# Kernel optimization log

Hardware: AMD Instinct MI355X
Metric: run time of the kernel (lower is better)

## Reference

```python
import jax, jax.numpy as jnp
import numpy as np

OUT_F = 4096   # compressed rows; logical m = 2*OUT_F
IN_F = 2048    # compressed cols; logical k = 2*IN_F
BATCH = 4096   # n = input.shape[0]

# valid sorted 2-of-4 column patterns for 2:4 structured sparsity
_PAIR_LUT = jnp.array([[0, 1], [0, 2], [0, 3], [1, 2], [1, 3], [2, 3]], dtype=jnp.int32)


def setup_inputs() -> dict:
    key = jax.random.key(0)
    k1, k2, k3, k4 = jax.random.split(key, 4)
    weight = jax.random.normal(k1, (OUT_F, IN_F), dtype=jnp.float32)
    # vector (row) sparsity: keep 1 of every 2 logical row-vectors -> collision-free logical row ids
    row_bit = jax.random.randint(k2, (OUT_F,), 0, 2)
    indices = (2 * jnp.arange(OUT_F, dtype=jnp.int32) + row_bit.astype(jnp.int32))
    # 2:4 column sparsity: per group of 4 logical cols, keep 2 distinct sorted positions
    pat = jax.random.randint(k3, (OUT_F, IN_F // 2), 0, 6)
    metadata = _PAIR_LUT[pat].reshape(OUT_F, IN_F)  # [OUT_F, IN_F], values in 0..3
    inp = jax.random.normal(k4, (BATCH, 2 * IN_F), dtype=jnp.float32)
    return {"weight": weight, "indices": indices, "metadata": metadata, "input": inp}


def reference(weight, indices, metadata, input):
    # Decompress the dual structured-sparse weight to its logical dense form,
    # then compute W_logical @ input^T (spmm_dense_trans semantics).
    out_f, in_f = weight.shape
    m, k = 2 * out_f, 2 * in_f
    # logical column of each compressed element: group base 4*(c//2) + 2-bit metadata
    col = 4 * (jnp.arange(in_f, dtype=jnp.int32) // 2)[None, :] + metadata  # [out_f, in_f]
    W = jnp.zeros((m, k), dtype=weight.dtype).at[indices[:, None], col].set(weight)
    return W @ input.T  # [m, n] = [2*out_f, batch]
```

## Files before the change

kernel.cpp:

```cpp
#include <hip/hip_runtime.h>

#define OUT_F 4096
#define IN_F  2048
#define KLOG  4096
#define NB    4096
typedef unsigned long long ull;
typedef ull ullx2 __attribute__((ext_vector_type(2)));

typedef __bf16 bf16x8 __attribute__((ext_vector_type(8)));
typedef short  s16x8  __attribute__((ext_vector_type(8)));
typedef float  f32x4  __attribute__((ext_vector_type(4)));
typedef float  f32x16 __attribute__((ext_vector_type(16)));

__device__ __forceinline__ unsigned short f2bf(float f) {
    unsigned int u = __float_as_uint(f);
    u += 0x7fffu + ((u >> 16) & 1u);
    return (unsigned short)(u >> 16);
}

__device__ __forceinline__ void gload_lds16(const void* g, void* l) {
    __builtin_amdgcn_global_load_lds(
        (const __attribute__((address_space(1))) unsigned int*)g,
        (__attribute__((address_space(3))) unsigned int*)l, 16, 0, 0);
}

__global__ __launch_bounds__(256) void prep_kernel(
    const float* __restrict__ weight, const int* __restrict__ metadata,
    const float* __restrict__ input,
    unsigned short* __restrict__ wsA, unsigned short* __restrict__ wsB)
{
    const int b = blockIdx.x;
    if (b < 4096) {
        const int g = b * 256 + threadIdx.x;
        const int r = g >> 8;
        const int c = (g & 255) * 8;
        const size_t off = (size_t)r * IN_F + c;
        const float4 w0 = *(const float4*)(weight + off);
        const float4 w1 = *(const float4*)(weight + off + 4);
        const int4   m0 = *(const int4*)(metadata + off);
        const int4   m1 = *(const int4*)(metadata + off + 4);
        ullx2 v01, v23;
        v01.x = ((ull)f2bf(w0.x) << (m0.x * 16)) | ((ull)f2bf(w0.y) << (m0.y * 16));
        v01.y = ((ull)f2bf(w0.z) << (m0.z * 16)) | ((ull)f2bf(w0.w) << (m0.w * 16));
        v23.x = ((ull)f2bf(w1.x) << (m1.x * 16)) | ((ull)f2bf(w1.y) << (m1.y * 16));
        v23.y = ((ull)f2bf(w1.z) << (m1.z * 16)) | ((ull)f2bf(w1.w) << (m1.w * 16));
        ull* dst = (ull*)(wsA + (size_t)r * KLOG + 2 * c);
        *(ullx2*)(dst)     = v01;
        *(ullx2*)(dst + 2) = v23;
    } else {
        const int g = (b - 4096) * 256 + threadIdx.x;
        const size_t off = (size_t)g * 16;
        const float4 f0 = *(const float4*)(input + off);
        const float4 f1 = *(const float4*)(input + off + 4);
        const float4 f2 = *(const float4*)(input + off + 8);
        const float4 f3 = *(const float4*)(input + off + 12);
        ullx2 v01, v23;
        v01.x =  (ull)f2bf(f0.x) | ((ull)f2bf(f0.y) << 16) | ((ull)f2bf(f0.z) << 32) | ((ull)f2bf(f0.w) << 48);
        v01.y =  (ull)f2bf(f1.x) | ((ull)f2bf(f1.y) << 16) | ((ull)f2bf(f1.z) << 32) | ((ull)f2bf(f1.w) << 48);
        v23.x =  (ull)f2bf(f2.x) | ((ull)f2bf(f2.y) << 16) | ((ull)f2bf(f2.z) << 32) | ((ull)f2bf(f2.w) << 48);
        v23.y =  (ull)f2bf(f3.x) | ((ull)f2bf(f3.y) << 16) | ((ull)f2bf(f3.z) << 32) | ((ull)f2bf(f3.w) << 48);
        ull* dst = (ull*)(wsB + off);
        *(ullx2*)(dst)     = v01;
        *(ullx2*)(dst + 2) = v23;
    }
}

__global__ __launch_bounds__(256) void gemm_kernel(
    const unsigned short* __restrict__ wsA, const unsigned short* __restrict__ wsB,
    const int* __restrict__ indices, float* __restrict__ out)
{
    __shared__ __align__(16) unsigned short As[128 * 32];
    __shared__ __align__(16) unsigned short Bs[128 * 32];

    const int tid  = threadIdx.x;
    const int lane = tid & 63;
    const int wave = tid >> 6;
    const int wm   = wave >> 1;
    const int wn   = wave & 1;
    const int l31  = lane & 31;
    const int h    = lane >> 5;

    const int r0 = blockIdx.y * 128;
    const int b0 = blockIdx.x * 128;

    const int srow   = wave * 32 + (lane >> 2);
    const int scol16 = (lane & 3) ^ ((lane >> 3) & 3);
    const unsigned ldsOff = wave * 2048;
    const unsigned short* gA = wsA + (size_t)(r0 + srow) * KLOG + scol16 * 8;
    const unsigned short* gB = wsB + (size_t)(b0 + srow) * KLOG + scol16 * 8;

    f32x16 acc[2][2];
#pragma unroll
    for (int i = 0; i < 2; ++i)
#pragma unroll
        for (int j = 0; j < 2; ++j)
#pragma unroll
            for (int e = 0; e < 16; ++e) acc[i][j][e] = 0.f;

    for (int k0 = 0; k0 < KLOG; k0 += 32) {
        gload_lds16(gA + k0,             (char*)As + ldsOff);
        gload_lds16(gA + 16 * KLOG + k0, (char*)As + ldsOff + 1024);
        gload_lds16(gB + k0,             (char*)Bs + ldsOff);
        gload_lds16(gB + 16 * KLOG + k0, (char*)Bs + ldsOff + 1024);
        __syncthreads();

        bf16x8 a[2][2], b[2][2];
#pragma unroll
        for (int mi = 0; mi < 2; ++mi)
#pragma unroll
            for (int kh = 0; kh < 2; ++kh) {
                const int row = wm * 64 + mi * 32 + l31;
                const int phys = (kh * 2 + h) ^ ((row >> 1) & 3);
                a[mi][kh] = __builtin_bit_cast(bf16x8, *(const s16x8*)(As + row * 32 + phys * 8));
            }
#pragma unroll
        for (int nj = 0; nj < 2; ++nj)
#pragma unroll
            for (int kh = 0; kh < 2; ++kh) {
                const int row = wn * 64 + nj * 32 + l31;
                const int phys = (kh * 2 + h) ^ ((row >> 1) & 3);
                b[nj][kh] = __builtin_bit_cast(bf16x8, *(const s16x8*)(Bs + row * 32 + phys * 8));
            }

#pragma unroll
        for (int kh = 0; kh < 2; ++kh)
#pragma unroll
            for (int mi = 0; mi < 2; ++mi)
#pragma unroll
                for (int nj = 0; nj < 2; ++nj)
                    acc[mi][nj] = __builtin_amdgcn_mfma_f32_32x32x16_bf16(
                                      a[mi][kh], b[nj][kh], acc[mi][nj], 0, 0, 0);
        __syncthreads();
    }

#pragma unroll
    for (int mi = 0; mi < 2; ++mi) {
#pragma unroll
        for (int reg = 0; reg < 16; ++reg) {
            const int rloc = wm * 64 + mi * 32 + (reg & 3) + 8 * (reg >> 2) + 4 * h;
            const int L = indices[r0 + rloc];
            const size_t base  = (size_t)L * NB;
            const size_t baseZ = (size_t)(L ^ 1) * NB;
#pragma unroll
            for (int nj = 0; nj < 2; ++nj) {
                const int col = b0 + wn * 64 + nj * 32 + l31;
                out[base  + col] = acc[mi][nj][reg];
                out[baseZ + col] = 0.0f;
            }
        }
    }
}

__global__ __launch_bounds__(256) void spmm_dt_fallback(
    const float* __restrict__ weight, const int* __restrict__ indices,
    const int* __restrict__ metadata, const float* __restrict__ input,
    float* __restrict__ out)
{
    __shared__ __align__(16) unsigned short As[128][32];
    __shared__ __align__(16) unsigned short Bs[128][32];
    const int tid = threadIdx.x, lane = tid & 63, wave = tid >> 6;
    const int wm = wave >> 1, wn = wave & 1, l15 = lane & 15, quad = lane >> 4;
    const int r0 = blockIdx.y * 128, b0 = blockIdx.x * 128;
    f32x4 acc[4][4];
#pragma unroll
    for (int i = 0; i < 4; ++i)
#pragma unroll
        for (int j = 0; j < 4; ++j) acc[i][j] = (f32x4){0.f, 0.f, 0.f, 0.f};
    const int srow = tid >> 3, sgrp = tid & 7;
    for (int kk = 0; kk < KLOG / 32; ++kk) {
        const int c0 = kk * 16, k0 = kk * 32;
#pragma unroll
        for (int s = 0; s < 4; ++s) {
            const int row = srow + s * 32;
            const size_t off = (size_t)(r0 + row) * IN_F + c0 + 2 * sgrp;
            const float2 w = *(const float2*)(weight + off);
            const int2  md = *(const int2*)(metadata + off);
            *(ull*)(&As[row][4 * sgrp]) =
                ((ull)f2bf(w.x) << (md.x * 16)) | ((ull)f2bf(w.y) << (md.y * 16));
        }
#pragma unroll
        for (int s = 0; s < 4; ++s) {
            const int row = srow + s * 32;
            const float4 f = *(const float4*)(&input[(size_t)(b0 + row) * KLOG + k0 + sgrp * 4]);
            *(ull*)(&Bs[row][sgrp * 4]) =
                 (ull)f2bf(f.x) | ((ull)f2bf(f.y) << 16) |
                ((ull)f2bf(f.z) << 32) | ((ull)f2bf(f.w) << 48);
        }
        __syncthreads();
        bf16x8 a[4], b[4];
#pragma unroll
        for (int i = 0; i < 4; ++i)
            a[i] = __builtin_bit_cast(bf16x8, *(const s16x8*)(&As[wm * 64 + i * 16 + l15][quad * 8]));
#pragma unroll
        for (int j = 0; j < 4; ++j)
            b[j] = __builtin_bit_cast(bf16x8, *(const s16x8*)(&Bs[wn * 64 + j * 16 + l15][quad * 8]));
#pragma unroll
        for (int i = 0; i < 4; ++i)
#pragma unroll
            for (int j = 0; j < 4; ++j)
                acc[i][j] = __builtin_amdgcn_mfma_f32_16x16x32_bf16(a[i], b[j], acc[i][j], 0, 0, 0);
        __syncthreads();
    }
#pragma unroll
    for (int i = 0; i < 4; ++i)
#pragma unroll
        for (int t = 0; t < 4; ++t) {
            const int r = r0 + wm * 64 + i * 16 + quad * 4 + t;
            const int L = indices[r];
            const size_t base = (size_t)L * NB, baseZ = (size_t)(L ^ 1) * NB;
#pragma unroll
            for (int j = 0; j < 4; ++j) {
                const int col = b0 + wn * 64 + j * 16 + l15;
                out[base + col] = acc[i][j][t];
                out[baseZ + col] = 0.0f;
            }
        }
}

extern "C" void kernel_launch(void* const* d_in, const int* in_sizes, int n_in,
                              void* d_out, int out_size, void* d_ws, size_t ws_size,
                              hipStream_t stream) {
    const float* weight   = (const float*)d_in[0];
    const int*   indices  = (const int*)d_in[1];
    const int*   metadata = (const int*)d_in[2];
    const float* input    = (const float*)d_in[3];
    float*       out      = (float*)d_out;

    const size_t needA = (size_t)OUT_F * KLOG * 2;
    const size_t needB = (size_t)NB * KLOG * 2;
    if (ws_size >= needA + needB) {
        unsigned short* wsA = (unsigned short*)d_ws;
        unsigned short* wsB = wsA + (size_t)OUT_F * KLOG;
        prep_kernel<<<dim3(8192), dim3(256), 0, stream>>>(weight, metadata, input, wsA, wsB);
        gemm_kernel<<<dim3(NB / 128, OUT_F / 128), dim3(256), 0, stream>>>(wsA, wsB, indices, out);
    } else {
        spmm_dt_fallback<<<dim3(NB / 128, OUT_F / 128), dim3(256), 0, stream>>>(
            weight, indices, metadata, input, out);
    }
}
```

Baseline: 384.6 us.

## Replace GEMM with 256x256-tile, 8-wave, 4-stage pipelined LDS kernel

Replaces the 128x128-tile, 4-wave GEMM with a 256x256-tile kernel using 512 threads. It adds a 4-buffer LDS ring with loads issued three steps ahead, explicit vmcnt/lgkmcnt waits, and s_setprio around the MFMA groups. A swizzled block-to-tile mapping is added to improve L2 reuse across neighbouring blocks. The intent is to raise arithmetic intensity and hide global-load latency behind MFMA work. The cost is 128KB of LDS per block and only 256 blocks, which limits occupancy and depends on hand-tuned wait counts being correct.

```diff
diff --git a/kernel.cpp b/kernel.cpp
--- a/kernel.cpp
+++ b/kernel.cpp
@@ -23,6 +23,12 @@
         (const __attribute__((address_space(1))) unsigned int*)g,
         (__attribute__((address_space(3))) unsigned int*)l, 16, 0, 0);
 }
+
+__device__ __forceinline__ bf16x8 ldsf(const char* p) {
+    return __builtin_bit_cast(bf16x8, *(const s16x8*)p);
+}
+
+#define MFMA32(a, b, c) __builtin_amdgcn_mfma_f32_32x32x16_bf16((a), (b), (c), 0, 0, 0)
 
 __global__ __launch_bounds__(256) void prep_kernel(
     const float* __restrict__ weight, const int* __restrict__ metadata,
@@ -65,86 +71,136 @@
     }
 }
 
-__global__ __launch_bounds__(256) void gemm_kernel(
+__global__ __launch_bounds__(512, 2) void gemm_kernel256(
     const unsigned short* __restrict__ wsA, const unsigned short* __restrict__ wsB,
     const int* __restrict__ indices, float* __restrict__ out)
 {
-    __shared__ __align__(16) unsigned short As[128 * 32];
-    __shared__ __align__(16) unsigned short Bs[128 * 32];
+    __shared__ __align__(16) char lds[4 * 32768];
 
     const int tid  = threadIdx.x;
     const int lane = tid & 63;
     const int wave = tid >> 6;
-    const int wm   = wave >> 1;
-    const int wn   = wave & 1;
+    const int wm   = wave >> 2;
+    const int wn   = wave & 3;
     const int l31  = lane & 31;
     const int h    = lane >> 5;
 
-    const int r0 = blockIdx.y * 128;
-    const int b0 = blockIdx.x * 128;
-
-    const int srow   = wave * 32 + (lane >> 2);
-    const int scol16 = (lane & 3) ^ ((lane >> 3) & 3);
-    const unsigned ldsOff = wave * 2048;
-    const unsigned short* gA = wsA + (size_t)(r0 + srow) * KLOG + scol16 * 8;
-    const unsigned short* gB = wsB + (size_t)(b0 + srow) * KLOG + scol16 * 8;
-
-    f32x16 acc[2][2];
-#pragma unroll
-    for (int i = 0; i < 2; ++i)
+    const int swz = ((blockIdx.x & 7) << 5) | (blockIdx.x >> 3);
+    const int r0 = (swz >> 4) << 8;
+    const int b0 = (swz & 15) << 8;
+
+    const int srow   = tid >> 2;
+    const int schunk = (tid & 3) ^ ((tid >> 3) & 3);
+    const unsigned short* gA = wsA + (size_t)(r0 + srow) * KLOG + schunk * 8;
+    const unsigned short* gB = wsB + (size_t)(b0 + srow) * KLOG + schunk * 8;
+    char* const ldsW = lds + wave * 1024;
+
+    const int q = (l31 >> 1) & 3;
+    const unsigned x0 = (unsigned)(((0 + h) ^ q) * 16);
+    const unsigned x1 = (unsigned)(((2 + h) ^ q) * 16);
+    const unsigned aRow = (unsigned)((wm * 128 + l31) * 64);
+    const unsigned bRow = (unsigned)((wn * 64  + l31) * 64);
+
+    f32x16 acc[4][2];
+#pragma unroll
+    for (int i = 0; i < 4; ++i)
 #pragma unroll
         for (int j = 0; j < 2; ++j)
 #pragma unroll
             for (int e = 0; e < 16; ++e) acc[i][j][e] = 0.f;
 
-    for (int k0 = 0; k0 < KLOG; k0 += 32) {
-        gload_lds16(gA + k0,             (char*)As + ldsOff);
-        gload_lds16(gA + 16 * KLOG + k0, (char*)As + ldsOff + 1024);
-        gload_lds16(gB + k0,             (char*)Bs + ldsOff);
-        gload_lds16(gB + 16 * KLOG + k0, (char*)Bs + ldsOff + 1024);
-        __syncthreads();
-
-        bf16x8 a[2][2], b[2][2];
-#pragma unroll
-        for (int mi = 0; mi < 2; ++mi)
-#pragma unroll
-            for (int kh = 0; kh < 2; ++kh) {
-                const int row = wm * 64 + mi * 32 + l31;
-                const int phys = (kh * 2 + h) ^ ((row >> 1) & 3);
-                a[mi][kh] = __builtin_bit_cast(bf16x8, *(const s16x8*)(As + row * 32 + phys * 8));
-            }
-#pragma unroll
-        for (int nj = 0; nj < 2; ++nj)
-#pragma unroll
-            for (int kh = 0; kh < 2; ++kh) {
-                const int row = wn * 64 + nj * 32 + l31;
-                const int phys = (kh * 2 + h) ^ ((row >> 1) & 3);
-                b[nj][kh] = __builtin_bit_cast(bf16x8, *(const s16x8*)(Bs + row * 32 + phys * 8));
-            }
-
-#pragma unroll
-        for (int kh = 0; kh < 2; ++kh)
-#pragma unroll
-            for (int mi = 0; mi < 2; ++mi)
-#pragma unroll
-                for (int nj = 0; nj < 2; ++nj)
-                    acc[mi][nj] = __builtin_amdgcn_mfma_f32_32x32x16_bf16(
-                                      a[mi][kh], b[nj][kh], acc[mi][nj], 0, 0, 0);
-        __syncthreads();
-    }
-
-#pragma unroll
-    for (int mi = 0; mi < 2; ++mi) {
+#define STAGE_A(t_) do { \
+        char* _d = ldsW + (((t_) & 3) * 32768); \
+        const unsigned short* _s = gA + (t_) * 32; \
+        gload_lds16(_s, _d); \
+        gload_lds16(_s + (size_t)128 * KLOG, _d + 8192); } while (0)
+#define STAGE_B(t_) do { \
+        char* _d = ldsW + (((t_) & 3) * 32768) + 16384; \
+        const unsigned short* _s = gB + (t_) * 32; \
+        gload_lds16(_s, _d); \
+        gload_lds16(_s + (size_t)128 * KLOG, _d + 8192); } while (0)
+
+    STAGE_A(0); STAGE_B(0);
+    STAGE_A(1); STAGE_B(1);
+    STAGE_A(2); STAGE_B(2);
+    asm volatile("s_waitcnt vmcnt(8)" ::: "memory");
+    __builtin_amdgcn_s_barrier();
+    __builtin_amdgcn_sched_barrier(0);
+
+    for (int t = 0; t < 128; ++t) {
+        const unsigned bufA = (unsigned)(t & 3) * 32768u;
+        const char* pA = lds + bufA + aRow;
+        const char* pB = lds + bufA + 16384u + bRow;
+
+        bf16x8 a0 = ldsf(pA + x0);
+        bf16x8 a1 = ldsf(pA + 2048 + x0);
+        bf16x8 a2 = ldsf(pA + 4096 + x0);
+        bf16x8 a3 = ldsf(pA + 6144 + x0);
+        bf16x8 bb0 = ldsf(pB + x0);
+        bf16x8 bb1 = ldsf(pB + 2048 + x0);
+        if (t < 125) STAGE_A(t + 3);
+        __builtin_amdgcn_s_barrier();
+        asm volatile("s_waitcnt lgkmcnt(0)" ::: "memory");
+        __builtin_amdgcn_sched_barrier(0);
+        __builtin_amdgcn_s_setprio(1);
+        acc[0][0] = MFMA32(a0, bb0, acc[0][0]);
+        acc[0][1] = MFMA32(a0, bb1, acc[0][1]);
+        acc[1][0] = MFMA32(a1, bb0, acc[1][0]);
+        acc[1][1] = MFMA32(a1, bb1, acc[1][1]);
+        acc[2][0] = MFMA32(a2, bb0, acc[2][0]);
+        acc[2][1] = MFMA32(a2, bb1, acc[2][1]);
+        acc[3][0] = MFMA32(a3, bb0, acc[3][0]);
+        acc[3][1] = MFMA32(a3, bb1, acc[3][1]);
+        __builtin_amdgcn_s_setprio(0);
+        __builtin_amdgcn_sched_barrier(0);
+
+        a0 = ldsf(pA + x1);
+        a1 = ldsf(pA + 2048 + x1);
+        a2 = ldsf(pA + 4096 + x1);
+        a3 = ldsf(pA + 6144 + x1);
+        bb0 = ldsf(pB + x1);
+        bb1 = ldsf(pB + 2048 + x1);
+        if (t < 125) STAGE_B(t + 3);
+        __builtin_amdgcn_s_barrier();
+        asm volatile("s_waitcnt lgkmcnt(0)" ::: "memory");
+        __builtin_amdgcn_sched_barrier(0);
+        __builtin_amdgcn_s_setprio(1);
+        acc[0][0] = MFMA32(a0, bb0, acc[0][0]);
+        acc[0][1] = MFMA32(a0, bb1, acc[0][1]);
+        acc[1][0] = MFMA32(a1, bb0, acc[1][0]);
+        acc[1][1] = MFMA32(a1, bb1, acc[1][1]);
+        acc[2][0] = MFMA32(a2, bb0, acc[2][0]);
+        acc[3][0] = MFMA32(a3, bb0, acc[3][0]);
+        acc[2][1] = MFMA32(a2, bb1, acc[2][1]);
+        acc[3][1] = MFMA32(a3, bb1, acc[3][1]);
+        __builtin_amdgcn_s_setprio(0);
+        __builtin_amdgcn_sched_barrier(0);
+
+        if (t < 125) {
+            asm volatile("s_waitcnt vmcnt(8)" ::: "memory");
+        } else if (t == 125) {
+            asm volatile("s_waitcnt vmcnt(4)" ::: "memory");
+        } else if (t == 126) {
+            asm volatile("s_waitcnt vmcnt(0)" ::: "memory");
+        }
+        __builtin_amdgcn_s_barrier();
+        __builtin_amdgcn_sched_barrier(0);
+    }
+#undef STAGE_A
+#undef STAGE_B
+
+#pragma unroll
+    for (int fm = 0; fm < 4; ++fm) {
 #pragma unroll
         for (int reg = 0; reg < 16; ++reg) {
-            const int rloc = wm * 64 + mi * 32 + (reg & 3) + 8 * (reg >> 2) + 4 * h;
+            const int rloc = wm * 128 + fm * 32 + (reg & 3) + 8 * (reg >> 2) + 4 * h;
             const int L = indices[r0 + rloc];
             const size_t base  = (size_t)L * NB;
             const size_t baseZ = (size_t)(L ^ 1) * NB;
 #pragma unroll
-            for (int nj = 0; nj < 2; ++nj) {
-                const int col = b0 + wn * 64 + nj * 32 + l31;
-                out[base  + col] = acc[mi][nj][reg];
+            for (int fn = 0; fn < 2; ++fn) {
+                const int col = b0 + wn * 64 + fn * 32 + l31;
+                out[base  + col] = acc[fm][fn][reg];
                 out[baseZ + col] = 0.0f;
             }
         }
@@ -232,7 +288,7 @@
         unsigned short* wsA = (unsigned short*)d_ws;
         unsigned short* wsB = wsA + (size_t)OUT_F * KLOG;
         prep_kernel<<<dim3(8192), dim3(256), 0, stream>>>(weight, metadata, input, wsA, wsB);
-        gemm_kernel<<<dim3(NB / 128, OUT_F / 128), dim3(256), 0, stream>>>(wsA, wsB, indices, out);
+        gemm_kernel256<<<dim3(256), dim3(512), 0, stream>>>(wsA, wsB, indices, out);
     } else {
         spmm_dt_fallback<<<dim3(NB / 128, OUT_F / 128), dim3(256), 0, stream>>>(
             weight, indices, metadata, input, out);
```

Measured after the change: 362.5 us. 1.06x faster.
